# Kernel optimization log

Hardware: AMD Instinct MI355X
Metric: run time of the kernel (lower is better)

The kernel has to match this reference:

```python
import jax, jax.numpy as jnp
import numpy as np

N = 100000      # nodes
E = 1600000     # edges
G = 64          # graphs in batch
D_IN, D_H, D_OUT = 128, 128, 64


def setup_inputs() -> dict:
    key = jax.random.key(0)
    k1, k2, k3, k4, k5, k6, k7 = jax.random.split(key, 7)
    x = jax.random.normal(k1, (N, D_IN), dtype=jnp.float32)
    edge_index = jax.random.randint(k2, (2, E), 0, N, dtype=jnp.int64)
    batch = jnp.sort(jax.random.randint(k3, (N,), 0, G, dtype=jnp.int64))
    # GCNConv params (glorot-ish scale)
    W1 = jax.random.normal(k4, (D_IN, D_H), dtype=jnp.float32) / np.sqrt(D_IN)
    b1 = jnp.zeros((D_H,), dtype=jnp.float32)
    W2 = jax.random.normal(k5, (D_H, D_OUT), dtype=jnp.float32) / np.sqrt(D_H)
    b2 = jnp.zeros((D_OUT,), dtype=jnp.float32)
    return {"x": x, "edge_index": edge_index, "batch": batch,
            "W1": W1, "b1": b1, "W2": W2, "b2": b2}


def gcn_conv(x, W, b, src, dst, n):
    # PyG GCNConv: linear transform, add self-loops, symmetric deg^-1/2 norm,
    # gather messages from src, scatter-add into dst, add bias.
    xw = x @ W  # [n, d_out]
    ones = jnp.ones(src.shape[0], dtype=xw.dtype)
    deg = jax.ops.segment_sum(ones, dst, num_segments=n)  # includes self-loop
    dinv = jnp.where(deg > 0, jax.lax.rsqrt(deg), 0.0)
    norm = dinv[src] * dinv[dst]                      # [e_total]
    msg = xw[src] * norm[:, None]                     # gather + scale
    out = jax.ops.segment_sum(msg, dst, num_segments=n)  # scatter-add
    return out + b


def reference(x, edge_index, batch, W1, b1, W2, b2):
    n = x.shape[0]
    loops = jnp.arange(n, dtype=edge_index.dtype)
    src = jnp.concatenate([edge_index[0], loops])  # self-loops appended
    dst = jnp.concatenate([edge_index[1], loops])
    h = jax.nn.relu(gcn_conv(x, W1, b1, src, dst, n))
    h = jax.nn.relu(gcn_conv(h, W2, b2, src, dst, n))
    # global_mean_pool over graph ids
    sums = jax.ops.segment_sum(h, batch, num_segments=G)          # [G, d]
    cnt = jax.ops.segment_sum(jnp.ones((n,), h.dtype), batch, num_segments=G)
    return sums / jnp.maximum(cnt, 1.0)[:, None]
```

## Files before the change

### kernel.cpp

```cpp
#include <hip/hip_runtime.h>
#include <hip/hip_bf16.h>


#define DIN 128
#define DH  128
#define DOUTC 64

__device__ inline unsigned short f2bf(float f) {
    union { float f; unsigned u; } v; v.f = f;
    unsigned r = v.u + 0x7FFF + ((v.u >> 16) & 1);
    return (unsigned short)(r >> 16);
}
__device__ inline float bf_lo(unsigned u) { return __uint_as_float(u << 16); }
__device__ inline float bf_hi(unsigned u) { return __uint_as_float(u & 0xFFFF0000u); }


__global__ void zero_i32_kernel(int* __restrict__ p, int n) {
    int i = blockIdx.x * blockDim.x + threadIdx.x;
    if (i < n) p[i] = 0;
}

__global__ void zero_f32_kernel(float* __restrict__ p, int n) {
    int i = blockIdx.x * blockDim.x + threadIdx.x;
    if (i < n) p[i] = 0.0f;
}

__global__ void deg_count_kernel(int* __restrict__ cnt, const int* __restrict__ dst,
                                 int* __restrict__ rank, int e) {
    int i = blockIdx.x * blockDim.x + threadIdx.x;
    if (i < e) rank[i] = atomicAdd(&cnt[dst[i]], 1);
}

__global__ __launch_bounds__(256) void scan1_kernel(const int* __restrict__ deg,
                                                    int* __restrict__ excl,
                                                    int* __restrict__ blockSums,
                                                    float* __restrict__ dinv, int n) {
    __shared__ int sh[256];
    const int tid = threadIdx.x;
    const int base = blockIdx.x * 1024 + tid * 4;
    int v[4];
    #pragma unroll
    for (int j = 0; j < 4; ++j) v[j] = (base + j < n) ? deg[base + j] : 0;
    #pragma unroll
    for (int j = 0; j < 4; ++j)
        if (base + j < n) dinv[base + j] = rsqrtf((float)(v[j] + 1));
    int tsum = v[0] + v[1] + v[2] + v[3];
    sh[tid] = tsum;
    __syncthreads();
    for (int off = 1; off < 256; off <<= 1) {
        int add = (tid >= off) ? sh[tid - off] : 0;
        __syncthreads();
        sh[tid] += add;
        __syncthreads();
    }
    int texcl = sh[tid] - tsum;
    int run = texcl;
    #pragma unroll
    for (int j = 0; j < 4; ++j) {
        if (base + j < n) excl[base + j] = run;
        run += v[j];
    }
    if (tid == 255) blockSums[blockIdx.x] = sh[255];
}

__global__ void scan2_kernel(int* __restrict__ blockSums, int nb) {
    if (blockIdx.x == 0 && threadIdx.x == 0) {
        int run = 0;
        for (int i = 0; i < nb; ++i) {
            int t = blockSums[i];
            blockSums[i] = run;
            run += t;
        }
    }
}

__global__ void scan3_kernel(int* __restrict__ row_ptr, const int* __restrict__ blockSums,
                             int n, int e_total) {
    int i = blockIdx.x * blockDim.x + threadIdx.x;
    if (i < n) row_ptr[i] += blockSums[i >> 10];
    if (i == 0) row_ptr[n] = e_total;
}

__global__ void scatter_kernel(const int* __restrict__ src, const int* __restrict__ dst,
                               const int* __restrict__ rank, const float* __restrict__ dinv,
                               const int* __restrict__ row_ptr,
                               int2* __restrict__ ep, int e_total) {
    int e = blockIdx.x * blockDim.x + threadIdx.x;
    if (e >= e_total) return;
    int s = src[e];
    int d = dst[e];
    int r = rank[e];
    float ds = dinv[s];
    float dd = dinv[d];
    int pos = row_ptr[d] + r;
    ep[pos] = make_int2(s, __float_as_int(ds * dd));
}

template <int DOUT>
__global__ __launch_bounds__(256) void gemm_k128_bf16out(const float* __restrict__ X,
                                                         const float* __restrict__ W,
                                                         unsigned short* __restrict__ Y, int n) {
    constexpr int K = 128;
    constexpr int TR = 64;
    constexpr int COLV = DOUT / 4;
    constexpr int RS = 256 / COLV;
    constexpr int RPT = TR / RS;

    __shared__ float xs[TR][K];

    const int tid = threadIdx.x;
    const int row0 = blockIdx.x * TR;

    #pragma unroll
    for (int i = 0; i < 8; ++i) {
        int idx = i * 256 + tid;
        int r = idx >> 5;
        int c = idx & 31;
        int gr = row0 + r;
        float4 v = make_float4(0.f, 0.f, 0.f, 0.f);
        if (gr < n) v = reinterpret_cast<const float4*>(X)[(size_t)gr * 32 + c];
        reinterpret_cast<float4*>(&xs[0][0])[idx] = v;
    }
    __syncthreads();

    const int col = tid % COLV;
    const int rslot = tid / COLV;

    float4 acc[RPT];
    #pragma unroll
    for (int r = 0; r < RPT; ++r) acc[r] = make_float4(0.f, 0.f, 0.f, 0.f);

    #pragma unroll 4
    for (int k = 0; k < K; ++k) {
        float4 w = reinterpret_cast<const float4*>(W)[k * COLV + col];
        #pragma unroll
        for (int r = 0; r < RPT; ++r) {
            float xv = xs[rslot + r * RS][k];
            acc[r].x += xv * w.x;
            acc[r].y += xv * w.y;
            acc[r].z += xv * w.z;
            acc[r].w += xv * w.w;
        }
    }

    #pragma unroll
    for (int r = 0; r < RPT; ++r) {
        int gr = row0 + rslot + r * RS;
        if (gr < n) {
            ushort4 st;
            st.x = f2bf(acc[r].x);
            st.y = f2bf(acc[r].y);
            st.z = f2bf(acc[r].z);
            st.w = f2bf(acc[r].w);
            reinterpret_cast<ushort4*>(Y)[(size_t)gr * COLV + col] = st;
        }
    }
}

template <int D>
__global__ __launch_bounds__(256) void agg_relu_kernel(const unsigned short* __restrict__ XW,
                                                       const int2* __restrict__ ep,
                                                       const int* __restrict__ row_ptr,
                                                       const float* __restrict__ dinv,
                                                       const float* __restrict__ bias,
                                                       float* __restrict__ OUT, int n) {
    const int tid = threadIdx.x;
    const int node = (blockIdx.x * 256 + tid) >> 6;
    const int lane = tid & 63;
    if (node >= n) return;

    const int start = row_ptr[node];
    const int end = row_ptr[node + 1];

    if constexpr (D == 128) {
        const unsigned* XWu = reinterpret_cast<const unsigned*>(XW);
        float di = dinv[node];
        float sl = di * di;
        unsigned rv = XWu[(size_t)node * 64 + lane];
        float ax = bf_lo(rv) * sl, ay = bf_hi(rv) * sl;
        float bx = 0.f, by = 0.f;

        int p = start;
        for (; p + 8 <= end; p += 8) {
            int2 m0 = ep[p + 0]; int2 m1 = ep[p + 1];
            int2 m2 = ep[p + 2]; int2 m3 = ep[p + 3];
            int2 m4 = ep[p + 4]; int2 m5 = ep[p + 5];
            int2 m6 = ep[p + 6]; int2 m7 = ep[p + 7];
            unsigned u0 = XWu[(size_t)m0.x * 64 + lane];
            unsigned u1 = XWu[(size_t)m1.x * 64 + lane];
            unsigned u2 = XWu[(size_t)m2.x * 64 + lane];
            unsigned u3 = XWu[(size_t)m3.x * 64 + lane];
            unsigned u4 = XWu[(size_t)m4.x * 64 + lane];
            unsigned u5 = XWu[(size_t)m5.x * 64 + lane];
            unsigned u6 = XWu[(size_t)m6.x * 64 + lane];
            unsigned u7 = XWu[(size_t)m7.x * 64 + lane];
            float w0 = __int_as_float(m0.y), w1 = __int_as_float(m1.y);
            float w2 = __int_as_float(m2.y), w3 = __int_as_float(m3.y);
            float w4 = __int_as_float(m4.y), w5 = __int_as_float(m5.y);
            float w6 = __int_as_float(m6.y), w7 = __int_as_float(m7.y);
            ax += bf_lo(u0) * w0; ay += bf_hi(u0) * w0;
            bx += bf_lo(u1) * w1; by += bf_hi(u1) * w1;
            ax += bf_lo(u2) * w2; ay += bf_hi(u2) * w2;
            bx += bf_lo(u3) * w3; by += bf_hi(u3) * w3;
            ax += bf_lo(u4) * w4; ay += bf_hi(u4) * w4;
            bx += bf_lo(u5) * w5; by += bf_hi(u5) * w5;
            ax += bf_lo(u6) * w6; ay += bf_hi(u6) * w6;
            bx += bf_lo(u7) * w7; by += bf_hi(u7) * w7;
        }
        for (; p + 4 <= end; p += 4) {
            int2 m0 = ep[p + 0]; int2 m1 = ep[p + 1];
            int2 m2 = ep[p + 2]; int2 m3 = ep[p + 3];
            unsigned u0 = XWu[(size_t)m0.x * 64 + lane];
            unsigned u1 = XWu[(size_t)m1.x * 64 + lane];
            unsigned u2 = XWu[(size_t)m2.x * 64 + lane];
            unsigned u3 = XWu[(size_t)m3.x * 64 + lane];
            float w0 = __int_as_float(m0.y), w1 = __int_as_float(m1.y);
            float w2 = __int_as_float(m2.y), w3 = __int_as_float(m3.y);
            ax += bf_lo(u0) * w0; ay += bf_hi(u0) * w0;
            bx += bf_lo(u1) * w1; by += bf_hi(u1) * w1;
            ax += bf_lo(u2) * w2; ay += bf_hi(u2) * w2;
            bx += bf_lo(u3) * w3; by += bf_hi(u3) * w3;
        }
        for (; p < end; ++p) {
            int2 m = ep[p];
            float w = __int_as_float(m.y);
            unsigned u = XWu[(size_t)m.x * 64 + lane];
            ax += bf_lo(u) * w;
            ay += bf_hi(u) * w;
        }
        ax += bx; ay += by;

        float2 b = reinterpret_cast<const float2*>(bias)[lane];
        float2 o;
        o.x = fmaxf(ax + b.x, 0.f);
        o.y = fmaxf(ay + b.y, 0.f);
        reinterpret_cast<float2*>(OUT)[(size_t)node * 64 + lane] = o;
    } else {
        float di = dinv[node];
        float sl = di * di;
        float acc0 = __uint_as_float(((unsigned)XW[(size_t)node * D + lane]) << 16) * sl;
        float acc1 = 0.f;

        int p = start;
        for (; p + 8 <= end; p += 8) {
            int2 m0 = ep[p + 0]; int2 m1 = ep[p + 1];
            int2 m2 = ep[p + 2]; int2 m3 = ep[p + 3];
            int2 m4 = ep[p + 4]; int2 m5 = ep[p + 5];
            int2 m6 = ep[p + 6]; int2 m7 = ep[p + 7];
            float u0 = __uint_as_float(((unsigned)XW[(size_t)m0.x * D + lane]) << 16);
            float u1 = __uint_as_float(((unsigned)XW[(size_t)m1.x * D + lane]) << 16);
            float u2 = __uint_as_float(((unsigned)XW[(size_t)m2.x * D + lane]) << 16);
            float u3 = __uint_as_float(((unsigned)XW[(size_t)m3.x * D + lane]) << 16);
            float u4 = __uint_as_float(((unsigned)XW[(size_t)m4.x * D + lane]) << 16);
            float u5 = __uint_as_float(((unsigned)XW[(size_t)m5.x * D + lane]) << 16);
            float u6 = __uint_as_float(((unsigned)XW[(size_t)m6.x * D + lane]) << 16);
            float u7 = __uint_as_float(((unsigned)XW[(size_t)m7.x * D + lane]) << 16);
            acc0 += u0 * __int_as_float(m0.y);
            acc1 += u1 * __int_as_float(m1.y);
            acc0 += u2 * __int_as_float(m2.y);
            acc1 += u3 * __int_as_float(m3.y);
            acc0 += u4 * __int_as_float(m4.y);
            acc1 += u5 * __int_as_float(m5.y);
            acc0 += u6 * __int_as_float(m6.y);
            acc1 += u7 * __int_as_float(m7.y);
        }
        for (; p + 4 <= end; p += 4) {
            int2 m0 = ep[p + 0]; int2 m1 = ep[p + 1];
            int2 m2 = ep[p + 2]; int2 m3 = ep[p + 3];
            float u0 = __uint_as_float(((unsigned)XW[(size_t)m0.x * D + lane]) << 16);
            float u1 = __uint_as_float(((unsigned)XW[(size_t)m1.x * D + lane]) << 16);
            float u2 = __uint_as_float(((unsigned)XW[(size_t)m2.x * D + lane]) << 16);
            float u3 = __uint_as_float(((unsigned)XW[(size_t)m3.x * D + lane]) << 16);
            acc0 += u0 * __int_as_float(m0.y);
            acc1 += u1 * __int_as_float(m1.y);
            acc0 += u2 * __int_as_float(m2.y);
            acc1 += u3 * __int_as_float(m3.y);
        }
        for (; p < end; ++p) {
            int2 m = ep[p];
            acc0 += __uint_as_float(((unsigned)XW[(size_t)m.x * D + lane]) << 16) * __int_as_float(m.y);
        }
        acc0 += acc1;

        float o = fmaxf(acc0 + bias[lane], 0.f);
        OUT[(size_t)node * D + lane] = o;
    }
}

#define POOL_CHUNK 64

__global__ __launch_bounds__(256) void pool_seg_kernel(const float* __restrict__ H,
                                                       const int* __restrict__ batch,
                                                       float* __restrict__ sums,
                                                       float* __restrict__ cnt, int n) {
    const int wave = (blockIdx.x * 256 + threadIdx.x) >> 6;
    const int lane = threadIdx.x & 63;
    int i0 = wave * POOL_CHUNK;
    if (i0 >= n) return;
    int i1 = min(i0 + POOL_CHUNK, n);

    int g = batch[i0];
    float acc = 0.0f;
    int segn = 0;
    for (int i = i0; i < i1; ++i) {
        int gi = batch[i];
        if (gi != g) {
            unsafeAtomicAdd(&sums[g * DOUTC + lane], acc);
            if (lane == 0) unsafeAtomicAdd(&cnt[g], (float)segn);
            g = gi;
            acc = 0.0f;
            segn = 0;
        }
        acc += H[(size_t)i * DOUTC + lane];
        ++segn;
    }
    unsafeAtomicAdd(&sums[g * DOUTC + lane], acc);
    if (lane == 0) unsafeAtomicAdd(&cnt[g], (float)segn);
}

__global__ void pool_finish_kernel(const float* __restrict__ sums, const float* __restrict__ cnt,
                                   float* __restrict__ out, int g_total) {
    int t = blockIdx.x * blockDim.x + threadIdx.x;
    if (t >= g_total * DOUTC) return;
    int g = t >> 6;
    out[t] = sums[t] / fmaxf(cnt[g], 1.0f);
}


extern "C" void kernel_launch(void* const* d_in, const int* in_sizes, int n_in,
                              void* d_out, int out_size, void* d_ws, size_t ws_size,
                              hipStream_t stream) {
    const float* x    = (const float*)d_in[0];
    const int*   ei   = (const int*)d_in[1];
    const int*   batch= (const int*)d_in[2];
    const float* W1   = (const float*)d_in[3];
    const float* b1   = (const float*)d_in[4];
    const float* W2   = (const float*)d_in[5];
    const float* b2   = (const float*)d_in[6];
    float* out = (float*)d_out;

    const int N = in_sizes[0] / DIN;
    const int E = in_sizes[1] / 2;
    const int G = out_size / DOUTC;

    const int* esrc = ei;
    const int* edst = ei + E;

    char* ws = (char*)d_ws;
    size_t off = 0;
    auto alloc = [&](size_t bytes) -> void* {
        void* p = ws + off;
        off = (off + bytes + 255) & ~(size_t)255;
        return p;
    };
    float* dinv    = (float*)alloc((size_t)N * 4);
    int*   row_ptr = (int*)alloc((size_t)(N + 1) * 4);
    int*   deg     = (int*)alloc((size_t)N * 4);
    int*   rank    = (int*)alloc((size_t)E * 4);
    int*   blockSums = (int*)alloc(1024 * 4);
    int2*  epack   = (int2*)alloc((size_t)E * 8);
    unsigned short* xwbf = (unsigned short*)alloc((size_t)N * DH * 2);
    float* bufB    = (float*)alloc((size_t)N * DH * 4);
    float* sums    = (float*)alloc((size_t)G * DOUTC * 4 + (size_t)G * 4);
    float* cnt     = sums + G * DOUTC;

    const int B = 256;
    auto cdiv = [](long long a, long long b) { return (int)((a + b - 1) / b); };
    const int nScanBlocks = cdiv(N, 1024);

    zero_i32_kernel<<<cdiv(N, B), B, 0, stream>>>(deg, N);
    zero_f32_kernel<<<cdiv(G * DOUTC + G, B), B, 0, stream>>>(sums, G * DOUTC + G);
    deg_count_kernel<<<cdiv(E, B), B, 0, stream>>>(deg, edst, rank, E);
    scan1_kernel<<<nScanBlocks, B, 0, stream>>>(deg, row_ptr, blockSums, dinv, N);
    scan2_kernel<<<1, 64, 0, stream>>>(blockSums, nScanBlocks);
    scan3_kernel<<<cdiv(N, B), B, 0, stream>>>(row_ptr, blockSums, N, E);
    scatter_kernel<<<cdiv(E, B), B, 0, stream>>>(esrc, edst, rank, dinv, row_ptr, epack, E);

    gemm_k128_bf16out<DH><<<cdiv(N, 64), B, 0, stream>>>(x, W1, xwbf, N);
    agg_relu_kernel<DH><<<cdiv(N, 4), B, 0, stream>>>(xwbf, epack, row_ptr, dinv, b1, bufB, N);

    gemm_k128_bf16out<DOUTC><<<cdiv(N, 64), B, 0, stream>>>(bufB, W2, xwbf, N);
    agg_relu_kernel<DOUTC><<<cdiv(N, 4), B, 0, stream>>>(xwbf, epack, row_ptr, dinv, b2, bufB, N);

    const int nPoolWaves = cdiv(N, POOL_CHUNK);
    pool_seg_kernel<<<cdiv((long long)nPoolWaves * 64, B), B, 0, stream>>>(bufB, batch, sums, cnt, N);
    pool_finish_kernel<<<cdiv(G * DOUTC, B), B, 0, stream>>>(sums, cnt, out, G);
}
```

Baseline: 370.2 us.

## Fuse degree counting into first GEMM and store layer-1 activations as bf16

Merges the two zero-fill kernels into one init kernel. Folds the degree-count atomics into the first GEMM launch as extra blocks so both run concurrently, which removes a launch and lets the atomic work overlap the GEMM. Layer-1 aggregation now writes bf16 instead of fp32, and the second GEMM reads bf16 input. This halves the intermediate traffic at the cost of extra rounding error.

```diff
diff --git a/kernel.cpp b/kernel.cpp
--- a/kernel.cpp
+++ b/kernel.cpp
@@ -14,21 +14,78 @@
 __device__ inline float bf_lo(unsigned u) { return __uint_as_float(u << 16); }
 __device__ inline float bf_hi(unsigned u) { return __uint_as_float(u & 0xFFFF0000u); }
 
-
-__global__ void zero_i32_kernel(int* __restrict__ p, int n) {
+__global__ void init_kernel(int* __restrict__ deg, float* __restrict__ sums, int n, int m) {
     int i = blockIdx.x * blockDim.x + threadIdx.x;
-    if (i < n) p[i] = 0;
-}
-
-__global__ void zero_f32_kernel(float* __restrict__ p, int n) {
-    int i = blockIdx.x * blockDim.x + threadIdx.x;
-    if (i < n) p[i] = 0.0f;
-}
-
-__global__ void deg_count_kernel(int* __restrict__ cnt, const int* __restrict__ dst,
-                                 int* __restrict__ rank, int e) {
-    int i = blockIdx.x * blockDim.x + threadIdx.x;
-    if (i < e) rank[i] = atomicAdd(&cnt[dst[i]], 1);
+    if (i < n) deg[i] = 0;
+    if (i < m) sums[i] = 0.0f;
+}
+
+__global__ __launch_bounds__(256) void gemm1_deg_kernel(const float* __restrict__ X,
+                                                        const float* __restrict__ W,
+                                                        unsigned short* __restrict__ Y, int n,
+                                                        const int* __restrict__ dst,
+                                                        int* __restrict__ deg,
+                                                        int* __restrict__ rank,
+                                                        int e_total, int nG) {
+    __shared__ float xs[64][128];
+    const int tid = threadIdx.x;
+
+    if ((int)blockIdx.x >= nG) {
+        int i = ((int)blockIdx.x - nG) * 256 + tid;
+        if (i < e_total) rank[i] = atomicAdd(&deg[dst[i]], 1);
+        return;
+    }
+
+    constexpr int COLV = 32;
+    constexpr int RS = 8;
+    constexpr int RPT = 8;
+
+    const int row0 = (int)blockIdx.x * 64;
+
+    #pragma unroll
+    for (int i = 0; i < 8; ++i) {
+        int idx = i * 256 + tid;
+        int r = idx >> 5;
+        int c = idx & 31;
+        int gr = row0 + r;
+        float4 v = make_float4(0.f, 0.f, 0.f, 0.f);
+        if (gr < n) v = reinterpret_cast<const float4*>(X)[(size_t)gr * 32 + c];
+        reinterpret_cast<float4*>(&xs[0][0])[idx] = v;
+    }
+    __syncthreads();
+
+    const int col = tid % COLV;
+    const int rslot = tid / COLV;
+
+    float4 acc[RPT];
+    #pragma unroll
+    for (int r = 0; r < RPT; ++r) acc[r] = make_float4(0.f, 0.f, 0.f, 0.f);
+
+    #pragma unroll 4
+    for (int k = 0; k < 128; ++k) {
+        float4 w = reinterpret_cast<const float4*>(W)[k * COLV + col];
+        #pragma unroll
+        for (int r = 0; r < RPT; ++r) {
+            float xv = xs[rslot + r * RS][k];
+            acc[r].x += xv * w.x;
+            acc[r].y += xv * w.y;
+            acc[r].z += xv * w.z;
+            acc[r].w += xv * w.w;
+        }
+    }
+
+    #pragma unroll
+    for (int r = 0; r < RPT; ++r) {
+        int gr = row0 + rslot + r * RS;
+        if (gr < n) {
+            ushort4 st;
+            st.x = f2bf(acc[r].x);
+            st.y = f2bf(acc[r].y);
+            st.z = f2bf(acc[r].z);
+            st.w = f2bf(acc[r].w);
+            reinterpret_cast<ushort4*>(Y)[(size_t)gr * COLV + col] = st;
+        }
+    }
 }
 
 __global__ __launch_bounds__(256) void scan1_kernel(const int* __restrict__ deg,
@@ -97,29 +154,30 @@
 }
 
 template <int DOUT>
-__global__ __launch_bounds__(256) void gemm_k128_bf16out(const float* __restrict__ X,
-                                                         const float* __restrict__ W,
-                                                         unsigned short* __restrict__ Y, int n) {
-    constexpr int K = 128;
-    constexpr int TR = 64;
+__global__ __launch_bounds__(256) void gemm_k128_bf16in(const unsigned short* __restrict__ X,
+                                                        const float* __restrict__ W,
+                                                        unsigned short* __restrict__ Y, int n) {
     constexpr int COLV = DOUT / 4;
     constexpr int RS = 256 / COLV;
-    constexpr int RPT = TR / RS;
-
-    __shared__ float xs[TR][K];
+    constexpr int RPT = 64 / RS;
+
+    __shared__ float xs[64][128];
 
     const int tid = threadIdx.x;
-    const int row0 = blockIdx.x * TR;
-
-    #pragma unroll
-    for (int i = 0; i < 8; ++i) {
+    const int row0 = (int)blockIdx.x * 64;
+
+    #pragma unroll
+    for (int i = 0; i < 4; ++i) {
         int idx = i * 256 + tid;
-        int r = idx >> 5;
-        int c = idx & 31;
-        int gr = row0 + r;
-        float4 v = make_float4(0.f, 0.f, 0.f, 0.f);
-        if (gr < n) v = reinterpret_cast<const float4*>(X)[(size_t)gr * 32 + c];
-        reinterpret_cast<float4*>(&xs[0][0])[idx] = v;
+        int r = idx >> 4;
+        int c8 = idx & 15;
+        uint4 v = make_uint4(0, 0, 0, 0);
+        if (row0 + r < n) v = reinterpret_cast<const uint4*>(X)[(size_t)(row0 + r) * 16 + c8];
+        float* dp = &xs[r][c8 * 8];
+        dp[0] = bf_lo(v.x); dp[1] = bf_hi(v.x);
+        dp[2] = bf_lo(v.y); dp[3] = bf_hi(v.y);
+        dp[4] = bf_lo(v.z); dp[5] = bf_hi(v.z);
+        dp[6] = bf_lo(v.w); dp[7] = bf_hi(v.w);
     }
     __syncthreads();
 
@@ -131,7 +189,7 @@
     for (int r = 0; r < RPT; ++r) acc[r] = make_float4(0.f, 0.f, 0.f, 0.f);
 
     #pragma unroll 4
-    for (int k = 0; k < K; ++k) {
+    for (int k = 0; k < 128; ++k) {
         float4 w = reinterpret_cast<const float4*>(W)[k * COLV + col];
         #pragma unroll
         for (int r = 0; r < RPT; ++r) {
@@ -157,13 +215,13 @@
     }
 }
 
-template <int D>
+template <int D, bool BFOUT>
 __global__ __launch_bounds__(256) void agg_relu_kernel(const unsigned short* __restrict__ XW,
                                                        const int2* __restrict__ ep,
                                                        const int* __restrict__ row_ptr,
                                                        const float* __restrict__ dinv,
                                                        const float* __restrict__ bias,
-                                                       float* __restrict__ OUT, int n) {
+                                                       void* __restrict__ OUT, int n) {
     const int tid = threadIdx.x;
     const int node = (blockIdx.x * 256 + tid) >> 6;
     const int lane = tid & 63;
@@ -231,10 +289,14 @@
         ax += bx; ay += by;
 
         float2 b = reinterpret_cast<const float2*>(bias)[lane];
-        float2 o;
-        o.x = fmaxf(ax + b.x, 0.f);
-        o.y = fmaxf(ay + b.y, 0.f);
-        reinterpret_cast<float2*>(OUT)[(size_t)node * 64 + lane] = o;
+        float ox = fmaxf(ax + b.x, 0.f);
+        float oy = fmaxf(ay + b.y, 0.f);
+        if constexpr (BFOUT) {
+            unsigned o = ((unsigned)f2bf(oy) << 16) | (unsigned)f2bf(ox);
+            reinterpret_cast<unsigned*>(OUT)[(size_t)node * 64 + lane] = o;
+        } else {
+            reinterpret_cast<float2*>(OUT)[(size_t)node * 64 + lane] = make_float2(ox, oy);
+        }
     } else {
         float di = dinv[node];
         float sl = di * di;
@@ -283,7 +345,7 @@
         acc0 += acc1;
 
         float o = fmaxf(acc0 + bias[lane], 0.f);
-        OUT[(size_t)node * D + lane] = o;
+        reinterpret_cast<float*>(OUT)[(size_t)node * D + lane] = o;
     }
 }
 
@@ -360,27 +422,30 @@
     int*   blockSums = (int*)alloc(1024 * 4);
     int2*  epack   = (int2*)alloc((size_t)E * 8);
     unsigned short* xwbf = (unsigned short*)alloc((size_t)N * DH * 2);
-    float* bufB    = (float*)alloc((size_t)N * DH * 4);
+    unsigned short* h1bf = (unsigned short*)alloc((size_t)N * DH * 2);
+    float* bufB    = (float*)alloc((size_t)N * DOUTC * 4);
     float* sums    = (float*)alloc((size_t)G * DOUTC * 4 + (size_t)G * 4);
     float* cnt     = sums + G * DOUTC;
 
     const int B = 256;
     auto cdiv = [](long long a, long long b) { return (int)((a + b - 1) / b); };
     const int nScanBlocks = cdiv(N, 1024);
-
-    zero_i32_kernel<<<cdiv(N, B), B, 0, stream>>>(deg, N);
-    zero_f32_kernel<<<cdiv(G * DOUTC + G, B), B, 0, stream>>>(sums, G * DOUTC + G);
-    deg_count_kernel<<<cdiv(E, B), B, 0, stream>>>(deg, edst, rank, E);
+    const int nG = cdiv(N, 64);
+    const int nD = cdiv(E, B);
+    const int initM = G * DOUTC + G;
+
+    init_kernel<<<cdiv(N > initM ? N : initM, B), B, 0, stream>>>(deg, sums, N, initM);
+    gemm1_deg_kernel<<<nG + nD, B, 0, stream>>>(x, W1, xwbf, N, edst, deg, rank, E, nG);
+
     scan1_kernel<<<nScanBlocks, B, 0, stream>>>(deg, row_ptr, blockSums, dinv, N);
     scan2_kernel<<<1, 64, 0, stream>>>(blockSums, nScanBlocks);
     scan3_kernel<<<cdiv(N, B), B, 0, stream>>>(row_ptr, blockSums, N, E);
     scatter_kernel<<<cdiv(E, B), B, 0, stream>>>(esrc, edst, rank, dinv, row_ptr, epack, E);
 
-    gemm_k128_bf16out<DH><<<cdiv(N, 64), B, 0, stream>>>(x, W1, xwbf, N);
-    agg_relu_kernel<DH><<<cdiv(N, 4), B, 0, stream>>>(xwbf, epack, row_ptr, dinv, b1, bufB, N);
-
-    gemm_k128_bf16out<DOUTC><<<cdiv(N, 64), B, 0, stream>>>(bufB, W2, xwbf, N);
-    agg_relu_kernel<DOUTC><<<cdiv(N, 4), B, 0, stream>>>(xwbf, epack, row_ptr, dinv, b2, bufB, N);
+    agg_relu_kernel<DH, true><<<cdiv(N, 4), B, 0, stream>>>(xwbf, epack, row_ptr, dinv, b1, h1bf, N);
+
+    gemm_k128_bf16in<DOUTC><<<nG, B, 0, stream>>>(h1bf, W2, xwbf, N);
+    agg_relu_kernel<DOUTC, false><<<cdiv(N, 4), B, 0, stream>>>(xwbf, epack, row_ptr, dinv, b2, bufB, N);
 
     const int nPoolWaves = cdiv(N, POOL_CHUNK);
     pool_seg_kernel<<<cdiv((long long)nPoolWaves * 64, B), B, 0, stream>>>(bufB, batch, sums, cnt, N);
```

Result: faster. 339.6 us (-8.3%).
